# Performance work log

Hardware: AMD Instinct MI355X
Metric: run time of the kernel (lower is better)

The kernel has to match this reference:

```python
import jax, jax.numpy as jnp
import numpy as np

N_USERS = 100000
N_ITEMS = 100000
NNZ = 3200000
D = 128

def _spmm(rows, cols, vals, dense, n_out):
    # COO SpMM: out[r] += vals * dense[c]
    gathered = dense[cols] * vals[:, None]  # [nnz, D]
    return jax.ops.segment_sum(gathered, rows, num_segments=n_out)

def setup_inputs() -> dict:
    key = jax.random.key(0)
    ks = jax.random.split(key, 7)
    return {
        "input": jax.random.normal(ks[0], (N_USERS + N_ITEMS, D), dtype=jnp.float32),
        "user_rows": jax.random.randint(ks[1], (NNZ,), 0, N_USERS, dtype=jnp.int32),
        "user_cols": jax.random.randint(ks[2], (NNZ,), 0, N_USERS, dtype=jnp.int32),
        "user_vals": jax.random.uniform(ks[3], (NNZ,), dtype=jnp.float32),
        "item_rows": jax.random.randint(ks[4], (NNZ,), 0, N_ITEMS, dtype=jnp.int32),
        "item_cols": jax.random.randint(ks[5], (NNZ,), 0, N_ITEMS, dtype=jnp.int32),
        "item_vals": jax.random.uniform(ks[6], (NNZ,), dtype=jnp.float32),
    }

def reference(input, user_rows, user_cols, user_vals, item_rows, item_cols, item_vals):
    users_emb = input[:N_USERS]          # [n_users, D]
    items_emb = input[N_USERS:]          # [n_items, D]
    h_u1 = _spmm(user_rows, user_cols, user_vals, users_emb, N_USERS)
    h_i1 = _spmm(item_rows, item_cols, item_vals, items_emb, N_ITEMS)
    return jnp.concatenate([h_u1, h_i1], axis=0)
```

## Files before the change

### kernel.cpp

```cpp
#include <hip/hip_runtime.h>

#define NU    100000
#define NI    100000
#define NNZE  3200000
#define D     128

#define SROWS 512
#define SEGS  196
#define NSEG  392
#define CAPA  18432
#define STG   32
#define CAPL  64
#define OVFCAP 65536

typedef unsigned long long u64;

__device__ __forceinline__ unsigned bf16r(float x) {
    unsigned u = __float_as_uint(x);
    return (u + 0x7FFFu + ((u >> 16) & 1u)) >> 16;
}
__device__ __forceinline__ void push_ovf(u64* __restrict__ ovf, int* __restrict__ ovfcnt,
                                         int row, int col, unsigned vbits, int side) {
    int p = atomicAdd(ovfcnt, 1);
    if (p < OVFCAP) {
        ovf[p] = (u64)(unsigned)row
               | ((u64)(unsigned)col << 17)
               | ((u64)(((vbits + 0x8000u) >> 16) & 0xFFFFu) << 34)
               | ((u64)(unsigned)side << 50);
    }
}

__global__ void cvt_kernel(const float* __restrict__ in, unsigned short* __restrict__ outb) {
    const int total = (NU + NI) * D / 8;
    int gid = blockIdx.x * blockDim.x + threadIdx.x;
    const int stride = gridDim.x * blockDim.x;
    for (int i = gid; i < total; i += stride) {
        const float4 a = reinterpret_cast<const float4*>(in)[2 * i];
        const float4 b = reinterpret_cast<const float4*>(in)[2 * i + 1];
        uint4 w;
        w.x = bf16r(a.x) | (bf16r(a.y) << 16);
        w.y = bf16r(a.z) | (bf16r(a.w) << 16);
        w.z = bf16r(b.x) | (bf16r(b.y) << 16);
        w.w = bf16r(b.z) | (bf16r(b.w) << 16);
        reinterpret_cast<uint4*>(outb)[i] = w;
    }
}

__global__ __launch_bounds__(512) void phaseA_kernel(
        const int* __restrict__ urows, const int* __restrict__ ucols,
        const float* __restrict__ uvals,
        const int* __restrict__ irows, const int* __restrict__ icols,
        const float* __restrict__ ivals,
        int* __restrict__ cur, u64* __restrict__ appends,
        u64* __restrict__ ovf, int* __restrict__ ovfcnt) {
    __shared__ u64 stage[NSEG * STG];
    __shared__ int scnt[NSEG];
    for (int b = threadIdx.x; b < NSEG; b += 512) scnt[b] = 0;
    __syncthreads();

    const int nth  = gridDim.x * 512;
    const int gid0 = blockIdx.x * 512 + threadIdx.x;
    const int rounds = (NNZE + nth - 1) / nth;

    for (int rd = 0; rd < rounds; ++rd) {
        const int e = rd * nth + gid0;
        if (e < NNZE) {
            {
                const int r = urows[e], c = ucols[e];
                const unsigned vb = __float_as_uint(uvals[e]);
                const int b = r >> 9;
                const int p = atomicAdd(&scnt[b], 1);
                const u64 ent = ((u64)vb << 32) | ((u64)(unsigned)c << 9) | (unsigned)(r & 511);
                if (p < STG) stage[b * STG + p] = ent;
                else push_ovf(ovf, ovfcnt, r, c, vb, 0);
            }
            {
                const int r = irows[e], c = icols[e];
                const unsigned vb = __float_as_uint(ivals[e]);
                const int b = SEGS + (r >> 9);
                const int p = atomicAdd(&scnt[b], 1);
                const u64 ent = ((u64)vb << 32) | ((u64)(unsigned)c << 9) | (unsigned)(r & 511);
                if (p < STG) stage[b * STG + p] = ent;
                else push_ovf(ovf, ovfcnt, r, c, vb, 1);
            }
        }
        __syncthreads();
        if (threadIdx.x < NSEG) {
            const int b = threadIdx.x;
            int c = scnt[b]; if (c > STG) c = STG;
            const int nf = c & ~15;
            if (nf) {
                const int base = atomicAdd(&cur[b], nf);
                for (int k = 0; k < nf; ++k) {
                    const int idx = base + k;
                    const u64 ent = stage[b * STG + k];
                    if (idx < CAPA) {
                        appends[(size_t)b * CAPA + idx] = ent;
                    } else {
                        const int side = (b >= SEGS) ? 1 : 0;
                        push_ovf(ovf, ovfcnt,
                                 (((b - side * SEGS) << 9) | (int)(ent & 511u)),
                                 (int)((ent >> 9) & 0x1FFFFu), (unsigned)(ent >> 32), side);
                    }
                }
                for (int k = 0; k < c - nf; ++k) stage[b * STG + k] = stage[b * STG + nf + k];
                c -= nf;
            }
            scnt[b] = c;
        }
        __syncthreads();
    }
    if (threadIdx.x < NSEG) {
        const int b = threadIdx.x;
        int c = scnt[b]; if (c > STG) c = STG;
        if (c) {
            const int base = atomicAdd(&cur[b], c);
            for (int k = 0; k < c; ++k) {
                const int idx = base + k;
                const u64 ent = stage[b * STG + k];
                if (idx < CAPA) {
                    appends[(size_t)b * CAPA + idx] = ent;
                } else {
                    const int side = (b >= SEGS) ? 1 : 0;
                    push_ovf(ovf, ovfcnt,
                             (((b - side * SEGS) << 9) | (int)(ent & 511u)),
                             (int)((ent >> 9) & 0x1FFFFu), (unsigned)(ent >> 32), side);
                }
            }
        }
    }
}

__global__ __launch_bounds__(256) void phaseB_kernel(
        const int* __restrict__ cur, u64* __restrict__ appends,
        int* __restrict__ cntG, u64* __restrict__ ovf, int* __restrict__ ovfcnt) {
    __shared__ int cnt[SROWS];
    __shared__ unsigned bins[SROWS * CAPL];
    const int seg = blockIdx.x;
    const int side = (seg >= SEGS) ? 1 : 0;
    const int seg_side = seg - side * SEGS;

    for (int i = threadIdx.x; i < SROWS; i += 256) cnt[i] = 0;
    __syncthreads();

    int na = cur[seg]; if (na > CAPA) na = CAPA;
    u64* abase = appends + (size_t)seg * CAPA;
    for (int t = threadIdx.x; t < na; t += 256) {
        const u64 ent = abase[t];
        const int rl  = (int)(ent & 511u);
        const int col = (int)((ent >> 9) & 0x1FFFFu);
        const unsigned vb = (unsigned)(ent >> 32);
        const int p = atomicAdd(&cnt[rl], 1);
        if (p < CAPL) bins[(rl << 6) + p] = ((unsigned)col << 15) | (((vb + 0x8000u) >> 16) & 0x7FFFu);
        else push_ovf(ovf, ovfcnt, (seg_side << 9) + rl, col, vb, side);
    }
    __syncthreads();

    for (int r = threadIdx.x; r < SROWS; r += 256) {
        int c = cnt[r]; if (c > CAPL) c = CAPL;
        const int p = (c + 15) & ~15;
        for (int k = c; k < p; ++k) bins[(r << 6) + k] = 0u;
        cnt[r] = p;
    }
    __syncthreads();

    uint4* gb = reinterpret_cast<uint4*>(abase);
    const uint4* lb = reinterpret_cast<const uint4*>(bins);
    for (int i = threadIdx.x; i < SROWS * CAPL / 4; i += 256) gb[i] = lb[i];

    int* cbase = cntG + side * (SEGS * SROWS) + (seg_side << 9);
    for (int i = threadIdx.x; i < SROWS; i += 256) cbase[i] = cnt[i];
}

__global__ void pull_bf16_kernel(const unsigned short* __restrict__ tabb,
                                 const int* __restrict__ cntG,
                                 const u64* __restrict__ appends,
                                 float* __restrict__ out) {
    const int wid = (int)(((size_t)blockIdx.x * blockDim.x + threadIdx.x) >> 6);
    if (wid >= NU + NI) return;
    const int lane = threadIdx.x & 63;
    const int q    = lane >> 4;
    const int s16  = lane & 15;
    const int side = (wid >= NU) ? 1 : 0;
    const int row  = wid - side * NU;
    const unsigned short* src = tabb + (size_t)side * NU * D;
    float* dst = out + (size_t)side * NU * D;

    const int n = cntG[side * (SEGS * SROWS) + row];
    const int gseg = side * SEGS + (row >> 9);
    const unsigned* brow =
        reinterpret_cast<const unsigned*>(appends + (size_t)gseg * CAPA) + ((row & 511) << 6);

    float acc[8];
#pragma unroll
    for (int k = 0; k < 8; ++k) acc[k] = 0.f;

    const unsigned ent = brow[lane];
    const int   c = (int)(ent >> 15);
    const float v = __uint_as_float((ent & 0x7FFFu) << 16);

    for (int j = 0; j < n; j += 16) {
        int cc[4]; float vv[4]; uint4 x[4];
#pragma unroll
        for (int t = 0; t < 4; ++t) {
            const int jj = j + 4 * t + q;
            cc[t] = __shfl(c, jj); vv[t] = __shfl(v, jj);
        }
#pragma unroll
        for (int t = 0; t < 4; ++t) {
            x[t] = reinterpret_cast<const uint4*>(src + (size_t)cc[t] * D)[s16];
        }
#pragma unroll
        for (int t = 0; t < 4; ++t) {
#pragma unroll
            for (int w = 0; w < 4; ++w) {
                const unsigned u = (&x[t].x)[w];
                acc[2*w]   += __uint_as_float(u << 16)         * vv[t];
                acc[2*w+1] += __uint_as_float(u & 0xFFFF0000u) * vv[t];
            }
        }
    }
#pragma unroll
    for (int k = 0; k < 8; ++k) {
        acc[k] += __shfl_xor(acc[k], 16);
        acc[k] += __shfl_xor(acc[k], 32);
    }
    if (q == 0) {
        float4 o0, o1;
        o0.x = acc[0]; o0.y = acc[1]; o0.z = acc[2]; o0.w = acc[3];
        o1.x = acc[4]; o1.y = acc[5]; o1.z = acc[6]; o1.w = acc[7];
        float4* op = reinterpret_cast<float4*>(dst + (size_t)row * D + 8 * s16);
        op[0] = o0; op[1] = o1;
    }
}

__global__ void tail_ovf_kernel(const float* __restrict__ input,
                                const u64* __restrict__ ovf,
                                const int* __restrict__ ovfcnt,
                                float* __restrict__ out) {
    int cntv = *ovfcnt;
    if (cntv > OVFCAP) cntv = OVFCAP;
    const long long total = (long long)cntv * 64;
    long long gid = (long long)blockIdx.x * blockDim.x + threadIdx.x;
    const long long stride = (long long)gridDim.x * blockDim.x;
    for (; gid < total; gid += stride) {
        const int e    = (int)(gid >> 6);
        const int lane = (int)(gid & 63);
        const u64 en = ovf[e];
        const int row  = (int)(en & 0x1FFFFu);
        const int col  = (int)((en >> 17) & 0x1FFFFu);
        const float v  = __uint_as_float((unsigned)((en >> 34) & 0xFFFFu) << 16);
        const int side = (int)((en >> 50) & 1u);
        const float* s = input + (size_t)side * NU * D;
        float*       d = out   + (size_t)side * NU * D;
        atomicAdd(&d[(size_t)row * D + 2 * lane],     s[(size_t)col * D + 2 * lane]     * v);
        atomicAdd(&d[(size_t)row * D + 2 * lane + 1], s[(size_t)col * D + 2 * lane + 1] * v);
    }
}

__global__ void hist_kernel(const int* __restrict__ urows,
                            const int* __restrict__ irows,
                            int* __restrict__ cnt_u, int* __restrict__ cnt_i) {
    int gid = blockIdx.x * blockDim.x + threadIdx.x;
    int stride = gridDim.x * blockDim.x;
    for (int e = gid; e < NNZE; e += stride) {
        atomicAdd(&cnt_u[urows[e]], 1);
        atomicAdd(&cnt_i[irows[e]], 1);
    }
}

__global__ void scan_kernel(int* __restrict__ cnt_u, int* __restrict__ off_u,
                            int* __restrict__ cnt_i, int* __restrict__ off_i) {
    int* cnt = (blockIdx.x == 0) ? cnt_u : cnt_i;
    int* off = (blockIdx.x == 0) ? off_u : off_i;
    const int n = (blockIdx.x == 0) ? NU : NI;
    __shared__ int lds[1024];
    int carry = 0;
    for (int base = 0; base < n; base += 1024) {
        const int i = base + (int)threadIdx.x;
        const int v = (i < n) ? cnt[i] : 0;
        lds[threadIdx.x] = v;
        __syncthreads();
        for (int ofs = 1; ofs < 1024; ofs <<= 1) {
            int t = (threadIdx.x >= (unsigned)ofs) ? lds[threadIdx.x - ofs] : 0;
            __syncthreads();
            lds[threadIdx.x] += t;
            __syncthreads();
        }
        const int incl = lds[threadIdx.x];
        const int excl = incl - v;
        if (i < n) {
            off[i] = carry + excl;
            cnt[i] = carry + excl;
        }
        carry += lds[1023];
        __syncthreads();
    }
    if (threadIdx.x == 0) off[n] = carry;
}

__global__ void scatter_kernel(const int* __restrict__ urows,
                               const int* __restrict__ irows,
                               int* __restrict__ cur_u, int* __restrict__ cur_i,
                               int* __restrict__ perm_u, int* __restrict__ perm_i) {
    int gid = blockIdx.x * blockDim.x + threadIdx.x;
    int stride = gridDim.x * blockDim.x;
    for (int e = gid; e < NNZE; e += stride) {
        int p = atomicAdd(&cur_u[urows[e]], 1);
        perm_u[p] = e;
        p = atomicAdd(&cur_i[irows[e]], 1);
        perm_i[p] = e;
    }
}

__global__ void pull_csr_kernel(const float* __restrict__ input,
                                const int* __restrict__ ucols, const float* __restrict__ uvals,
                                const int* __restrict__ icols, const float* __restrict__ ivals,
                                const int* __restrict__ off_u, const int* __restrict__ perm_u,
                                const int* __restrict__ off_i, const int* __restrict__ perm_i,
                                float* __restrict__ out) {
    const int wid = (int)(((size_t)blockIdx.x * blockDim.x + threadIdx.x) >> 6);
    if (wid >= NU + NI) return;
    const int lane = threadIdx.x & 63;
    const int* off; const int* perm; const int* cols; const float* vals;
    const float* src; float* dst; int row;
    if (wid < NU) {
        off = off_u; perm = perm_u; cols = ucols; vals = uvals;
        src = input; dst = out; row = wid;
    } else {
        off = off_i; perm = perm_i; cols = icols; vals = ivals;
        src = input + (size_t)NU * D; dst = out + (size_t)NU * D; row = wid - NU;
    }
    const int s = off[row];
    const int n = off[row + 1] - s;
    float accx = 0.f, accy = 0.f;
    for (int base = 0; base < n; base += 64) {
        int m = n - base; if (m > 64) m = 64;
        int c = 0; float v = 0.f;
        if (lane < m) {
            const int nz = perm[s + base + lane];
            c = cols[nz];
            v = vals[nz];
        }
        for (int j = 0; j < m; ++j) {
            const int   cc = __shfl(c, j);
            const float vv = __shfl(v, j);
            const float2 x = reinterpret_cast<const float2*>(src + (size_t)cc * D)[lane];
            accx += x.x * vv; accy += x.y * vv;
        }
    }
    float2 o; o.x = accx; o.y = accy;
    reinterpret_cast<float2*>(dst + (size_t)row * D)[lane] = o;
}

__global__ void spmm_scatter_kernel(const float* __restrict__ input,
                                    const int* __restrict__ urows,
                                    const int* __restrict__ ucols,
                                    const float* __restrict__ uvals,
                                    const int* __restrict__ irows,
                                    const int* __restrict__ icols,
                                    const float* __restrict__ ivals,
                                    float* __restrict__ out) {
    const long long total = 2LL * NNZE * 32;
    long long gid = (long long)blockIdx.x * blockDim.x + threadIdx.x;
    const long long stride = (long long)gridDim.x * blockDim.x;
    for (; gid < total; gid += stride) {
        const int e = (int)(gid >> 5);
        const int qq = (int)(gid & 31);
        int row, col; float val; const float* src; float* dst;
        if (e < NNZE) {
            row = urows[e]; col = ucols[e]; val = uvals[e];
            src = input; dst = out;
        } else {
            const int e2 = e - NNZE;
            row = irows[e2]; col = icols[e2]; val = ivals[e2];
            src = input + (long long)NU * D; dst = out + (long long)NU * D;
        }
        const float4 v = reinterpret_cast<const float4*>(src + (long long)col * D)[qq];
        float* o = dst + (long long)row * D + (qq << 2);
        atomicAdd(o + 0, v.x * val);
        atomicAdd(o + 1, v.y * val);
        atomicAdd(o + 2, v.z * val);
        atomicAdd(o + 3, v.w * val);
    }
}

extern "C" void kernel_launch(void* const* d_in, const int* in_sizes, int n_in,
                              void* d_out, int out_size, void* d_ws, size_t ws_size,
                              hipStream_t stream) {
    const float* input = (const float*)d_in[0];
    const int*   urows = (const int*)d_in[1];
    const int*   ucols = (const int*)d_in[2];
    const float* uvals = (const float*)d_in[3];
    const int*   irows = (const int*)d_in[4];
    const int*   icols = (const int*)d_in[5];
    const float* ivals = (const float*)d_in[6];
    float*       out   = (float*)d_out;

    const size_t appends_b = (size_t)NSEG * CAPA * 8;
    const size_t ovf_b     = (size_t)OVFCAP * 8;
    const size_t cur_b     = ((size_t)(NSEG + 1) * 4 + 15) & ~(size_t)15;
    const size_t cnt_b     = (size_t)2 * SEGS * SROWS * 4;
    const size_t tabb_b    = (size_t)(NU + NI) * D * 2;
    const size_t need_t1   = appends_b + ovf_b + cur_b + cnt_b + tabb_b;

    const size_t need_csr = ((size_t)NU + NI + (NU + 1) + (NI + 1) + 2 * (size_t)NNZE) * 4;

    if (ws_size >= need_t1) {
        char* base = (char*)d_ws;
        u64* appends = (u64*)base;
        u64* ovf     = (u64*)(base + appends_b);
        int* cur     = (int*)(base + appends_b + ovf_b);
        int* ovfcnt  = cur + NSEG;
        int* cntG    = (int*)(base + appends_b + ovf_b + cur_b);
        unsigned short* tabb = (unsigned short*)(base + appends_b + ovf_b + cur_b + cnt_b);

        hipMemsetAsync(cur, 0, (size_t)(NSEG + 1) * sizeof(int), stream);
        phaseA_kernel<<<256, 512, 0, stream>>>(
            urows, ucols, uvals, irows, icols, ivals, cur, appends, ovf, ovfcnt);
        cvt_kernel<<<4096, 256, 0, stream>>>(input, tabb);
        phaseB_kernel<<<NSEG, 256, 0, stream>>>(cur, appends, cntG, ovf, ovfcnt);
        pull_bf16_kernel<<<(NU + NI + 3) / 4, 256, 0, stream>>>(tabb, cntG, appends, out);
        tail_ovf_kernel<<<64, 256, 0, stream>>>(input, ovf, ovfcnt, out);
    } else if (ws_size >= need_csr) {
        int* cur_u  = (int*)d_ws;
        int* cur_i  = cur_u + NU;
        int* off_u  = cur_i + NI;
        int* off_i  = off_u + (NU + 1);
        int* perm_u = off_i + (NI + 1);
        int* perm_i = perm_u + NNZE;

        hipMemsetAsync(cur_u, 0, (size_t)(NU + NI) * sizeof(int), stream);
        hist_kernel<<<2048, 256, 0, stream>>>(urows, irows, cur_u, cur_i);
        scan_kernel<<<2, 1024, 0, stream>>>(cur_u, off_u, cur_i, off_i);
        scatter_kernel<<<2048, 256, 0, stream>>>(urows, irows, cur_u, cur_i, perm_u, perm_i);
        pull_csr_kernel<<<(NU + NI + 3) / 4, 256, 0, stream>>>(
            input, ucols, uvals, icols, ivals, off_u, perm_u, off_i, perm_i, out);
    } else {
        hipMemsetAsync(out, 0, (size_t)out_size * sizeof(float), stream);
        spmm_scatter_kernel<<<8192, 256, 0, stream>>>(
            input, urows, ucols, uvals, irows, icols, ivals, out);
    }
}
```

Measured before the change: 512.5 us.

## Fuse bf16 conversion into phaseA and flush staged bins wave-parallel

```diff
diff --git a/kernel.cpp b/kernel.cpp
--- a/kernel.cpp
+++ b/kernel.cpp
@@ -9,7 +9,7 @@
 #define SEGS  196
 #define NSEG  392
 #define CAPA  18432
-#define STG   32
+#define STG   24
 #define CAPL  64
 #define OVFCAP 65536
 
@@ -30,33 +30,21 @@
     }
 }
 
-__global__ void cvt_kernel(const float* __restrict__ in, unsigned short* __restrict__ outb) {
-    const int total = (NU + NI) * D / 8;
-    int gid = blockIdx.x * blockDim.x + threadIdx.x;
-    const int stride = gridDim.x * blockDim.x;
-    for (int i = gid; i < total; i += stride) {
-        const float4 a = reinterpret_cast<const float4*>(in)[2 * i];
-        const float4 b = reinterpret_cast<const float4*>(in)[2 * i + 1];
-        uint4 w;
-        w.x = bf16r(a.x) | (bf16r(a.y) << 16);
-        w.y = bf16r(a.z) | (bf16r(a.w) << 16);
-        w.z = bf16r(b.x) | (bf16r(b.y) << 16);
-        w.w = bf16r(b.z) | (bf16r(b.w) << 16);
-        reinterpret_cast<uint4*>(outb)[i] = w;
-    }
-}
-
 __global__ __launch_bounds__(512) void phaseA_kernel(
         const int* __restrict__ urows, const int* __restrict__ ucols,
         const float* __restrict__ uvals,
         const int* __restrict__ irows, const int* __restrict__ icols,
         const float* __restrict__ ivals,
         int* __restrict__ cur, u64* __restrict__ appends,
-        u64* __restrict__ ovf, int* __restrict__ ovfcnt) {
+        u64* __restrict__ ovf, int* __restrict__ ovfcnt,
+        const float* __restrict__ input, unsigned short* __restrict__ tabb) {
     __shared__ u64 stage[NSEG * STG];
     __shared__ int scnt[NSEG];
     for (int b = threadIdx.x; b < NSEG; b += 512) scnt[b] = 0;
     __syncthreads();
+
+    const int wv = threadIdx.x >> 6;
+    const int ln = threadIdx.x & 63;
 
     const int nth  = gridDim.x * 512;
     const int gid0 = blockIdx.x * 512 + threadIdx.x;
@@ -85,15 +73,16 @@
             }
         }
         __syncthreads();
-        if (threadIdx.x < NSEG) {
-            const int b = threadIdx.x;
+        for (int b = wv; b < NSEG; b += 8) {
             int c = scnt[b]; if (c > STG) c = STG;
             const int nf = c & ~15;
             if (nf) {
-                const int base = atomicAdd(&cur[b], nf);
-                for (int k = 0; k < nf; ++k) {
-                    const int idx = base + k;
-                    const u64 ent = stage[b * STG + k];
+                int base0 = 0;
+                if (ln == 0) base0 = atomicAdd(&cur[b], nf);
+                base0 = __shfl(base0, 0);
+                if (ln < nf) {
+                    const u64 ent = stage[b * STG + ln];
+                    const int idx = base0 + ln;
                     if (idx < CAPA) {
                         appends[(size_t)b * CAPA + idx] = ent;
                     } else {
@@ -103,21 +92,24 @@
                                  (int)((ent >> 9) & 0x1FFFFu), (unsigned)(ent >> 32), side);
                     }
                 }
-                for (int k = 0; k < c - nf; ++k) stage[b * STG + k] = stage[b * STG + nf + k];
-                c -= nf;
+                const int rem = c - nf;
+                u64 moved = 0;
+                if (ln < rem) moved = stage[b * STG + nf + ln];
+                if (ln < rem) stage[b * STG + ln] = moved;
+                if (ln == 0) scnt[b] = rem;
             }
-            scnt[b] = c;
         }
         __syncthreads();
     }
-    if (threadIdx.x < NSEG) {
-        const int b = threadIdx.x;
+    for (int b = wv; b < NSEG; b += 8) {
         int c = scnt[b]; if (c > STG) c = STG;
         if (c) {
-            const int base = atomicAdd(&cur[b], c);
-            for (int k = 0; k < c; ++k) {
-                const int idx = base + k;
-                const u64 ent = stage[b * STG + k];
+            int base0 = 0;
+            if (ln == 0) base0 = atomicAdd(&cur[b], c);
+            base0 = __shfl(base0, 0);
+            if (ln < c) {
+                const u64 ent = stage[b * STG + ln];
+                const int idx = base0 + ln;
                 if (idx < CAPA) {
                     appends[(size_t)b * CAPA + idx] = ent;
                 } else {
@@ -128,6 +120,17 @@
                 }
             }
         }
+    }
+    const int total = (NU + NI) * D / 8;
+    for (int i = blockIdx.x * 512 + threadIdx.x; i < total; i += nth) {
+        const float4 a = reinterpret_cast<const float4*>(input)[2 * i];
+        const float4 b = reinterpret_cast<const float4*>(input)[2 * i + 1];
+        uint4 w;
+        w.x = bf16r(a.x) | (bf16r(a.y) << 16);
+        w.y = bf16r(a.z) | (bf16r(a.w) << 16);
+        w.z = bf16r(b.x) | (bf16r(b.y) << 16);
+        w.w = bf16r(b.z) | (bf16r(b.w) << 16);
+        reinterpret_cast<uint4*>(tabb)[i] = w;
     }
 }
 
@@ -416,9 +419,9 @@
         unsigned short* tabb = (unsigned short*)(base + appends_b + ovf_b + cur_b + cnt_b);
 
         hipMemsetAsync(cur, 0, (size_t)(NSEG + 1) * sizeof(int), stream);
-        phaseA_kernel<<<256, 512, 0, stream>>>(
-            urows, ucols, uvals, irows, icols, ivals, cur, appends, ovf, ovfcnt);
-        cvt_kernel<<<4096, 256, 0, stream>>>(input, tabb);
+        phaseA_kernel<<<512, 512, 0, stream>>>(
+            urows, ucols, uvals, irows, icols, ivals, cur, appends, ovf, ovfcnt,
+            input, tabb);
         phaseB_kernel<<<NSEG, 256, 0, stream>>>(cur, appends, cntG, ovf, ovfcnt);
         pull_bf16_kernel<<<(NU + NI + 3) / 4, 256, 0, stream>>>(tabb, cntG, appends, out);
         tail_ovf_kernel<<<64, 256, 0, stream>>>(input, ovf, ovfcnt, out);
```

Result: slower. 887.9 us (+73.3%).
